# Kernel tuning notes

Measured on AMD Instinct MI355X. Metric: run time of the kernel, lower is better.

Reference implementation:

```python
import jax, jax.numpy as jnp
import numpy as np

N_NODES = 10000
W_DIM = 512
N_EDGES = 200000


def setup_inputs() -> dict:
    key = jax.random.key(0)
    k1, k2, k3 = jax.random.split(key, 3)
    z_drug = jax.random.normal(k1, (N_NODES, W_DIM), dtype=jnp.float32)
    # glorot-style init for the bilinear weight
    glorot_std = jnp.sqrt(2.0 / (W_DIM + W_DIM)).astype(jnp.float32)
    weight = jax.random.normal(k2, (W_DIM, W_DIM), dtype=jnp.float32) * glorot_std
    batch_edges = jax.random.randint(k3, (2, N_EDGES), 0, N_NODES, dtype=jnp.int64)
    return {"z_drug": z_drug, "weight": weight, "batch_edges": batch_edges}


def reference(z_drug, weight, batch_edges):
    # edge_type == 'drug_drug': both endpoints come from the drug table.
    row_embed = z_drug[batch_edges[0]]  # [E, d]
    col_embed = z_drug[batch_edges[1]]  # [E, d]
    # score_e = row_e @ W @ col_e  == diag((Z1 W) Z2^T) without the N x N blowup
    score = jnp.einsum('ed,df,ef->e', row_embed, weight, col_embed)
    return jax.nn.sigmoid(score)  # is_sigmoid=True default
```

## Files before the change

### kernel.cpp

```cpp
#include <hip/hip_runtime.h>
#include <math.h>

#define DIM     512
#define NNODES  10000
#define NEDGES  200000
#define MPAD    10048
#define NMB     157
#define NGRP    5
#define NB      (NGRP * NNODES)
#define SCAN_BLK 49
#define GEMM_GRID (NMB * 4)

using short8  = __attribute__((ext_vector_type(8))) short;
using floatx4 = __attribute__((ext_vector_type(4))) float;
using half8   = __attribute__((ext_vector_type(8))) _Float16;
using half2v  = __attribute__((ext_vector_type(2))) _Float16;

__device__ inline float dot2acc(half2v a, half2v b, float c) {
#if __has_builtin(__builtin_amdgcn_fdot2)
    return __builtin_amdgcn_fdot2(a, b, c, false);
#else
    return fmaf((float)a[0], (float)b[0], fmaf((float)a[1], (float)b[1], c));
#endif
}

#define PREP_ZBLK 2512
__global__ __launch_bounds__(256) void prep(const float* __restrict__ Z,
                                            const float* __restrict__ W,
                                            _Float16* __restrict__ Zh16,
                                            _Float16* __restrict__ Wh16t,
                                            int* __restrict__ counts) {
    const int b = blockIdx.x;
    const int t = threadIdx.x;

    if (b < 196) {
        int i = b * 256 + t;
        if (i < NB) counts[i] = 0;
    }

    if (b < PREP_ZBLK) {
        const int idx8 = (b * 256 + t) * 8;
        const int m = idx8 >> 9;
        float x[8];
        if (m < NNODES) {
            float4 v0 = *(const float4*)(Z + idx8);
            float4 v1 = *(const float4*)(Z + idx8 + 4);
            x[0]=v0.x; x[1]=v0.y; x[2]=v0.z; x[3]=v0.w;
            x[4]=v1.x; x[5]=v1.y; x[6]=v1.z; x[7]=v1.w;
        } else {
            #pragma unroll
            for (int j = 0; j < 8; ++j) x[j] = 0.f;
        }
        half8 h;
        #pragma unroll
        for (int j = 0; j < 8; ++j) h[j] = (_Float16)x[j];
        *(half8*)(Zh16 + idx8) = h;
    } else {
        __shared__ float tile[64][65];
        const int wb = b - PREP_ZBLK;
        const int kb = (wb >> 3) * 64;
        const int nb = (wb & 7) * 64;
        const int kk = t >> 2;
        const int ch = t & 3;

        const float* src = W + (size_t)(kb + kk) * DIM + nb + ch * 16;
        #pragma unroll
        for (int q = 0; q < 4; ++q) {
            float4 v = *(const float4*)(src + q * 4);
            tile[kk][ch * 16 + q * 4 + 0] = v.x;
            tile[kk][ch * 16 + q * 4 + 1] = v.y;
            tile[kk][ch * 16 + q * 4 + 2] = v.z;
            tile[kk][ch * 16 + q * 4 + 3] = v.w;
        }
        __syncthreads();

        const int nn = kk;
        half8 h0, h1;
        #pragma unroll
        for (int i = 0; i < 8; ++i) h0[i] = (_Float16)tile[ch * 16 + i][nn];
        #pragma unroll
        for (int i = 0; i < 8; ++i) h1[i] = (_Float16)tile[ch * 16 + 8 + i][nn];
        _Float16* d = Wh16t + (size_t)(nb + nn) * DIM + kb + ch * 16;
        *(half8*)(d)     = h0;
        *(half8*)(d + 8) = h1;
    }
}

__global__ __launch_bounds__(256) void gemm_f16(const _Float16* __restrict__ Zh16,
                                                const _Float16* __restrict__ Wh16t,
                                                _Float16* __restrict__ ZWh,
                                                const int* __restrict__ eidx,
                                                int* __restrict__ counts) {
    __shared__ _Float16 Abuf[2][2 * 64 * 32];
    __shared__ _Float16 Bbuf[2][2 * 128 * 32];

    const int t     = threadIdx.x;
    const int bid   = blockIdx.x;
    const int n_idx = bid & 3;
    const int m0    = (bid >> 2) * 64;
    const int n0    = n_idx * 128;

    const int l  = t & 63;
    const int w  = t >> 6;
    const int wn = w * 32;
    const int lm = l & 15;
    const int lq = l >> 4;
    const unsigned wbase = (unsigned)(t & 192);

    floatx4 acc[4][2] = {};

    auto stage = [&](int buf, int k0) {
        #pragma unroll
        for (int p = 0; p < 2; ++p) {
            const int s   = p * 256 + t;
            const int kk  = s >> 8;
            const int row = (s >> 2) & 63;
            const int ch  = s & 3;
            const _Float16* src = Zh16 + (size_t)(m0 + row) * DIM + k0 + kk * 32 + ch * 8;
            __builtin_amdgcn_global_load_lds(
                (const __attribute__((address_space(1))) void*)src,
                (__attribute__((address_space(3))) void*)&Abuf[buf][(p * 256 + wbase) * 8],
                16, 0, 0);
        }
        #pragma unroll
        for (int p = 0; p < 4; ++p) {
            const int s   = p * 256 + t;
            const int kk  = s >> 9;
            const int row = (s >> 2) & 127;
            const int ch  = s & 3;
            const _Float16* src = Wh16t + (size_t)(n0 + row) * DIM + k0 + kk * 32 + ch * 8;
            __builtin_amdgcn_global_load_lds(
                (const __attribute__((address_space(1))) void*)src,
                (__attribute__((address_space(3))) void*)&Bbuf[buf][(p * 256 + wbase) * 8],
                16, 0, 0);
        }
    };

    stage(0, 0);
    __syncthreads();

    for (int s = 0; s < 8; ++s) {
        const int buf = s & 1;
        if (s < 7) stage(buf ^ 1, (s + 1) * 64);

        #pragma unroll
        for (int kk = 0; kk < 2; ++kk) {
            half8 aF[4], bF[2];
            #pragma unroll
            for (int i = 0; i < 4; ++i)
                aF[i] = *(const half8*)&Abuf[buf][kk * 2048 + (16 * i + lm) * 32 + lq * 8];
            #pragma unroll
            for (int j = 0; j < 2; ++j)
                bF[j] = *(const half8*)&Bbuf[buf][kk * 4096 + (wn + 16 * j + lm) * 32 + lq * 8];

            #pragma unroll
            for (int i = 0; i < 4; ++i)
                #pragma unroll
                for (int j = 0; j < 2; ++j)
                    acc[i][j] = __builtin_amdgcn_mfma_f32_16x16x32_f16(aF[i], bF[j], acc[i][j], 0, 0, 0);
        }

        __syncthreads();
    }

    #pragma unroll
    for (int i = 0; i < 4; ++i)
        #pragma unroll
        for (int j = 0; j < 2; ++j)
            #pragma unroll
            for (int r = 0; r < 4; ++r) {
                const int gm = m0 + 16 * i + lq * 4 + r;
                const int gn = n0 + wn + 16 * j + lm;
                if (gm < NNODES)
                    ZWh[(size_t)gm * DIM + gn] = (_Float16)acc[i][j][r];
            }

    for (int e = bid * 256 + t; e < NEDGES; e += GEMM_GRID * 256) {
        int r = eidx[e];
        int c = eidx[NEDGES + e];
        atomicAdd(&counts[(c >> 11) * NNODES + r], 1);
    }
}

__global__ __launch_bounds__(1024) void scan_local(const int* __restrict__ counts,
                                                   int* __restrict__ partial,
                                                   int* __restrict__ blksum) {
    __shared__ int wsum[16];
    __shared__ int woff[17];
    const int t    = threadIdx.x;
    const int lane = t & 63;
    const int wv   = t >> 6;
    const int i    = blockIdx.x * 1024 + t;

    int x = (i < NB) ? counts[i] : 0;

    int v = x;
    #pragma unroll
    for (int off = 1; off < 64; off <<= 1) {
        int u = __shfl_up(v, off, 64);
        if (lane >= off) v += u;
    }
    if (lane == 63) wsum[wv] = v;
    __syncthreads();
    if (t == 0) {
        int r = 0;
        #pragma unroll
        for (int k = 0; k < 16; ++k) { woff[k] = r; r += wsum[k]; }
        woff[16] = r;
    }
    __syncthreads();

    if (i < NB) partial[i] = woff[wv] + (v - x);
    if (t == 1023) blksum[blockIdx.x] = woff[16];
}

__global__ __launch_bounds__(1024) void scan_fix(const int* __restrict__ partial,
                                                 const int* __restrict__ blksum,
                                                 int* __restrict__ cursor) {
    __shared__ int base_s;
    const int t = threadIdx.x;
    const int b = blockIdx.x;

    if (t < 64) {
        int v = (t < b) ? blksum[t] : 0;
        #pragma unroll
        for (int off = 32; off > 0; off >>= 1)
            v += __shfl_xor(v, off, 64);
        if (t == 0) base_s = v;
    }
    __syncthreads();
    const int base = base_s;

    const int i = b * 1024 + t;
    if (i < NB)
        cursor[i] = base + partial[i];
}

__global__ void scatter_edges(const int* __restrict__ eidx,
                              int* __restrict__ cursor,
                              unsigned* __restrict__ keys,
                              unsigned short* __restrict__ rows16) {
    int e = blockIdx.x * blockDim.x + threadIdx.x;
    if (e < NEDGES) {
        int r = eidx[e];
        int c = eidx[NEDGES + e];
        int pos = atomicAdd(&cursor[(c >> 11) * NNODES + r], 1);
        keys[pos]   = ((unsigned)c << 18) | (unsigned)e;
        rows16[pos] = (unsigned short)r;
    }
}

__global__ __launch_bounds__(256) void edge_score_f(const _Float16* __restrict__ ZWh,
                                                    const _Float16* __restrict__ Zh,
                                                    const unsigned* __restrict__ keys,
                                                    const unsigned short* __restrict__ rows16,
                                                    float* __restrict__ out) {
    const int t    = threadIdx.x;
    const int wgid = blockIdx.x * 4 + (t >> 6);
    const int lane = t & 63;
    const int gq   = lane >> 4;
    const int sl   = lane & 15;

    const int ii = wgid * 4 + gq;
    const unsigned k = keys[ii];
    const int c = (int)(k >> 18);
    const int r = (int)rows16[ii];

    const _Float16* rp = ZWh + (size_t)r * DIM + sl * 32;
    const _Float16* cp = Zh  + (size_t)c * DIM + sl * 32;

    half8 ra0 = *(const half8*)(rp);
    half8 ra1 = *(const half8*)(rp + 8);
    half8 ra2 = *(const half8*)(rp + 16);
    half8 ra3 = *(const half8*)(rp + 24);
    half8 c0  = *(const half8*)(cp);
    half8 c1  = *(const half8*)(cp + 8);
    half8 c2  = *(const half8*)(cp + 16);
    half8 c3  = *(const half8*)(cp + 24);

    float s = 0.f;
    #pragma unroll
    for (int d = 0; d < 4; ++d) {
        s = dot2acc((half2v){ra0[2*d], ra0[2*d+1]}, (half2v){c0[2*d], c0[2*d+1]}, s);
        s = dot2acc((half2v){ra1[2*d], ra1[2*d+1]}, (half2v){c1[2*d], c1[2*d+1]}, s);
        s = dot2acc((half2v){ra2[2*d], ra2[2*d+1]}, (half2v){c2[2*d], c2[2*d+1]}, s);
        s = dot2acc((half2v){ra3[2*d], ra3[2*d+1]}, (half2v){c3[2*d], c3[2*d+1]}, s);
    }

    s += __shfl_xor(s, 1, 64);
    s += __shfl_xor(s, 2, 64);
    s += __shfl_xor(s, 4, 64);
    s += __shfl_xor(s, 8, 64);

    if (sl == 0)
        out[k & 0x3FFFFu] = 1.0f / (1.0f + expf(-s));
}

#define GTM 128
#define GTN 64
#define GTK 16
#define LDA 132
#define LDB 68

__global__ __launch_bounds__(256) void gemm_zw(const float* __restrict__ A,
                                               const float* __restrict__ B,
                                               float* __restrict__ C) {
    __shared__ float As[GTK * LDA];
    __shared__ float Bs[GTK * LDB];

    const int t  = threadIdx.x;
    const int m0 = blockIdx.x * GTM;
    const int n0 = blockIdx.y * GTN;
    const int tx = t & 15;
    const int ty = t >> 4;

    float acc[8][4] = {};

    for (int k0 = 0; k0 < DIM; k0 += GTK) {
        #pragma unroll
        for (int p = 0; p < 2; ++p) {
            int f  = t + p * 256;
            int mm = f >> 2;
            int kq = f & 3;
            int m  = m0 + mm;
            float4 v = make_float4(0.f, 0.f, 0.f, 0.f);
            if (m < NNODES)
                v = *(const float4*)(A + (size_t)m * DIM + k0 + kq * 4);
            As[(kq * 4 + 0) * LDA + mm] = v.x;
            As[(kq * 4 + 1) * LDA + mm] = v.y;
            As[(kq * 4 + 2) * LDA + mm] = v.z;
            As[(kq * 4 + 3) * LDA + mm] = v.w;
        }
        {
            int kb = t >> 4, n4 = t & 15;
            *(float4*)&Bs[kb * LDB + n4 * 4] =
                *(const float4*)(B + (size_t)(k0 + kb) * DIM + n0 + n4 * 4);
        }
        __syncthreads();

        #pragma unroll
        for (int kk = 0; kk < GTK; ++kk) {
            float4 a0 = *(const float4*)&As[kk * LDA + ty * 8];
            float4 a1 = *(const float4*)&As[kk * LDA + ty * 8 + 4];
            float4 b  = *(const float4*)&Bs[kk * LDB + tx * 4];
            float av[8] = {a0.x, a0.y, a0.z, a0.w, a1.x, a1.y, a1.z, a1.w};
            float bv[4] = {b.x, b.y, b.z, b.w};
            #pragma unroll
            for (int i = 0; i < 8; ++i)
                #pragma unroll
                for (int j = 0; j < 4; ++j)
                    acc[i][j] = fmaf(av[i], bv[j], acc[i][j]);
        }
        __syncthreads();
    }

    #pragma unroll
    for (int i = 0; i < 8; ++i) {
        int m = m0 + ty * 8 + i;
        if (m < NNODES)
            *(float4*)(C + (size_t)m * DIM + n0 + tx * 4) =
                make_float4(acc[i][0], acc[i][1], acc[i][2], acc[i][3]);
    }
}

__global__ __launch_bounds__(256) void edge_score(const float* __restrict__ ZW,
                                                  const float* __restrict__ Z,
                                                  const int* __restrict__ eidx,
                                                  float* __restrict__ out) {
    const int e    = blockIdx.x * 4 + (threadIdx.x >> 6);
    const int lane = threadIdx.x & 63;

    const int r = eidx[e];
    const int c = eidx[NEDGES + e];

    const float4* pr = (const float4*)(ZW + (size_t)r * DIM);
    const float4* pc = (const float4*)(Z  + (size_t)c * DIM);

    float4 a0 = pr[lane * 2 + 0];
    float4 a1 = pr[lane * 2 + 1];
    float4 b0 = pc[lane * 2 + 0];
    float4 b1 = pc[lane * 2 + 1];

    float s = a0.x * b0.x;
    s = fmaf(a0.y, b0.y, s);
    s = fmaf(a0.z, b0.z, s);
    s = fmaf(a0.w, b0.w, s);
    s = fmaf(a1.x, b1.x, s);
    s = fmaf(a1.y, b1.y, s);
    s = fmaf(a1.z, b1.z, s);
    s = fmaf(a1.w, b1.w, s);

    #pragma unroll
    for (int off = 32; off > 0; off >>= 1)
        s += __shfl_xor(s, off, 64);

    if (lane == 0)
        out[e] = 1.0f / (1.0f + expf(-s));
}

extern "C" void kernel_launch(void* const* d_in, const int* in_sizes, int n_in,
                              void* d_out, int out_size, void* d_ws, size_t ws_size,
                              hipStream_t stream) {
    const float* Z  = (const float*)d_in[0];
    const float* W  = (const float*)d_in[1];
    const int*   EI = (const int*)d_in[2];
    float* out = (float*)d_out;

    char* p = (char*)d_ws;
    _Float16* ZWh   = (_Float16*)p;  p += (size_t)MPAD * DIM * 2;
    _Float16* Zh16  = (_Float16*)p;  p += (size_t)MPAD * DIM * 2;
    _Float16* Wh16t = (_Float16*)p;  p += (size_t)DIM * DIM * 2;
    int* counts  = (int*)p;          p += (size_t)NB * 4;
    int* cursor  = (int*)p;          p += (size_t)NB * 4;
    int* partial = (int*)p;          p += (size_t)NB * 4;
    int* blksum  = (int*)p;          p += (size_t)SCAN_BLK * 4;
    unsigned* keys = (unsigned*)p;   p += (size_t)NEDGES * 4;
    unsigned short* rows16 = (unsigned short*)p; p += (size_t)NEDGES * 2;
    const size_t need_full = (size_t)(p - (char*)d_ws);

    if (ws_size >= need_full) {
        prep<<<PREP_ZBLK + 64, 256, 0, stream>>>(Z, W, Zh16, Wh16t, counts);
        gemm_f16<<<GEMM_GRID, 256, 0, stream>>>(Zh16, Wh16t, ZWh, EI, counts);
        scan_local<<<SCAN_BLK, 1024, 0, stream>>>(counts, partial, blksum);
        scan_fix<<<SCAN_BLK, 1024, 0, stream>>>(partial, blksum, cursor);
        scatter_edges<<<(NEDGES + 255) / 256, 256, 0, stream>>>(EI, cursor, keys, rows16);
        edge_score_f<<<NEDGES / 16, 256, 0, stream>>>(ZWh, Zh16, keys, rows16, out);
    } else {
        float* ZW = (float*)d_ws;
        dim3 g1((NNODES + GTM - 1) / GTM, DIM / GTN);
        gemm_zw<<<g1, 256, 0, stream>>>(Z, W, ZW);
        edge_score<<<NEDGES / 4, 256, 0, stream>>>(ZW, Z, EI, out);
    }
}
```

Measured before the change: 135.8 us.

## Fuse scan and edge scatter into one kernel with grid-wide spin barriers

Replaces the three kernels (local scan, scan fix-up, edge scatter) with a single 49-block kernel. Blocks coordinate through atomic counters and spin-wait barriers, and the flags are reset in the prep kernel. This removes two kernel launches and the partial-sum round trip. In exchange, the scatter of 200k edges now runs on only 49 blocks instead of many, and correctness depends on all blocks being co-resident.

```diff
diff --git a/kernel.cpp b/kernel.cpp
--- a/kernel.cpp
+++ b/kernel.cpp
@@ -8,7 +8,7 @@
 #define NMB     157
 #define NGRP    5
 #define NB      (NGRP * NNODES)
-#define SCAN_BLK 49
+#define SORT_BLK 49
 #define GEMM_GRID (NMB * 4)
 
 using short8  = __attribute__((ext_vector_type(8))) short;
@@ -29,7 +29,8 @@
                                             const float* __restrict__ W,
                                             _Float16* __restrict__ Zh16,
                                             _Float16* __restrict__ Wh16t,
-                                            int* __restrict__ counts) {
+                                            int* __restrict__ counts,
+                                            int* __restrict__ syncf) {
     const int b = blockIdx.x;
     const int t = threadIdx.x;
 
@@ -37,6 +38,7 @@
         int i = b * 256 + t;
         if (i < NB) counts[i] = 0;
     }
+    if (b == 196 && t < 2) syncf[t] = 0;
 
     if (b < PREP_ZBLK) {
         const int idx8 = (b * 256 + t) * 8;
@@ -182,18 +184,24 @@
     }
 }
 
-__global__ __launch_bounds__(1024) void scan_local(const int* __restrict__ counts,
-                                                   int* __restrict__ partial,
-                                                   int* __restrict__ blksum) {
+__global__ __launch_bounds__(1024) void sort_fused(const int* __restrict__ eidx,
+                                                   int* __restrict__ counts,
+                                                   int* __restrict__ blksum,
+                                                   int* __restrict__ cursor,
+                                                   unsigned* __restrict__ keys,
+                                                   unsigned short* __restrict__ rows16,
+                                                   int* __restrict__ syncf) {
     __shared__ int wsum[16];
     __shared__ int woff[17];
+    __shared__ int base_s;
+
     const int t    = threadIdx.x;
+    const int b    = blockIdx.x;
     const int lane = t & 63;
     const int wv   = t >> 6;
-    const int i    = blockIdx.x * 1024 + t;
+    const int i    = b * 1024 + t;
 
     int x = (i < NB) ? counts[i] : 0;
-
     int v = x;
     #pragma unroll
     for (int off = 1; off < 64; off <<= 1) {
@@ -207,41 +215,36 @@
         #pragma unroll
         for (int k = 0; k < 16; ++k) { woff[k] = r; r += wsum[k]; }
         woff[16] = r;
-    }
-    __syncthreads();
-
-    if (i < NB) partial[i] = woff[wv] + (v - x);
-    if (t == 1023) blksum[blockIdx.x] = woff[16];
-}
-
-__global__ __launch_bounds__(1024) void scan_fix(const int* __restrict__ partial,
-                                                 const int* __restrict__ blksum,
-                                                 int* __restrict__ cursor) {
-    __shared__ int base_s;
-    const int t = threadIdx.x;
-    const int b = blockIdx.x;
+        blksum[b] = r;
+    }
+    __syncthreads();
+    const int local_excl = woff[wv] + (v - x);
+
+    __threadfence();
+    if (t == 0) {
+        atomicAdd(&syncf[0], 1);
+        while (atomicAdd(&syncf[0], 0) < SORT_BLK) __builtin_amdgcn_s_sleep(1);
+    }
+    __syncthreads();
 
     if (t < 64) {
-        int v = (t < b) ? blksum[t] : 0;
+        int s = (t < b) ? atomicAdd(&blksum[t], 0) : 0;
         #pragma unroll
         for (int off = 32; off > 0; off >>= 1)
-            v += __shfl_xor(v, off, 64);
-        if (t == 0) base_s = v;
-    }
-    __syncthreads();
-    const int base = base_s;
-
-    const int i = b * 1024 + t;
-    if (i < NB)
-        cursor[i] = base + partial[i];
-}
-
-__global__ void scatter_edges(const int* __restrict__ eidx,
-                              int* __restrict__ cursor,
-                              unsigned* __restrict__ keys,
-                              unsigned short* __restrict__ rows16) {
-    int e = blockIdx.x * blockDim.x + threadIdx.x;
-    if (e < NEDGES) {
+            s += __shfl_xor(s, off, 64);
+        if (t == 0) base_s = s;
+    }
+    __syncthreads();
+    if (i < NB) cursor[i] = base_s + local_excl;
+
+    __threadfence();
+    if (t == 0) {
+        atomicAdd(&syncf[1], 1);
+        while (atomicAdd(&syncf[1], 0) < SORT_BLK) __builtin_amdgcn_s_sleep(1);
+    }
+    __syncthreads();
+
+    for (int e = i; e < NEDGES; e += SORT_BLK * 1024) {
         int r = eidx[e];
         int c = eidx[NEDGES + e];
         int pos = atomicAdd(&cursor[(c >> 11) * NNODES + r], 1);
@@ -412,18 +415,17 @@
     _Float16* Wh16t = (_Float16*)p;  p += (size_t)DIM * DIM * 2;
     int* counts  = (int*)p;          p += (size_t)NB * 4;
     int* cursor  = (int*)p;          p += (size_t)NB * 4;
-    int* partial = (int*)p;          p += (size_t)NB * 4;
-    int* blksum  = (int*)p;          p += (size_t)SCAN_BLK * 4;
+    int* blksum  = (int*)p;          p += (size_t)SORT_BLK * 4;
+    int* syncf   = (int*)p;          p += 16;
     unsigned* keys = (unsigned*)p;   p += (size_t)NEDGES * 4;
     unsigned short* rows16 = (unsigned short*)p; p += (size_t)NEDGES * 2;
     const size_t need_full = (size_t)(p - (char*)d_ws);
 
     if (ws_size >= need_full) {
-        prep<<<PREP_ZBLK + 64, 256, 0, stream>>>(Z, W, Zh16, Wh16t, counts);
+        prep<<<PREP_ZBLK + 64, 256, 0, stream>>>(Z, W, Zh16, Wh16t, counts, syncf);
         gemm_f16<<<GEMM_GRID, 256, 0, stream>>>(Zh16, Wh16t, ZWh, EI, counts);
-        scan_local<<<SCAN_BLK, 1024, 0, stream>>>(counts, partial, blksum);
-        scan_fix<<<SCAN_BLK, 1024, 0, stream>>>(partial, blksum, cursor);
-        scatter_edges<<<(NEDGES + 255) / 256, 256, 0, stream>>>(EI, cursor, keys, rows16);
+        sort_fused<<<SORT_BLK, 1024, 0, stream>>>(EI, counts, blksum, cursor,
+                                                  keys, rows16, syncf);
         edge_score_f<<<NEDGES / 16, 256, 0, stream>>>(ZWh, Zh16, keys, rows16, out);
     } else {
         float* ZW = (float*)d_ws;
```

After: 165.8 us. 1.22x slower.
